# Kernel tuning notes

Hardware: AMD Instinct MI355X
Metric: run time of the kernel (lower is better)

Reference implementation:

```python
import jax, jax.numpy as jnp
import numpy as np

N_TYPES = 4
N_REL = 8
N_HEADS = 8
IN_DIM = 256
N_HID = 128
D_K = N_HID // N_HEADS
N_LAYERS = 2
N_NODES = 100000
N_EDGES = 400000


def setup_inputs() -> dict:
    key = jax.random.key(0)
    ks = jax.random.split(key, 24)
    s = 0.05
    inp = {
        'node_feature': jax.random.normal(ks[0], (N_NODES, IN_DIM), jnp.float32),
        'node_type': jax.random.randint(ks[1], (N_NODES,), 0, N_TYPES),
        'edge_index': jax.random.randint(ks[2], (2, N_EDGES), 0, N_NODES),
        'edge_type': jax.random.randint(ks[3], (N_EDGES,), 0, N_REL),
        # per-type input adapters
        'adapt_w': jax.random.normal(ks[4], (N_TYPES, IN_DIM, N_HID), jnp.float32) * s,
        'adapt_b': jnp.zeros((N_TYPES, N_HID), jnp.float32),
        # HGT conv params, stacked over layers
        'k_w': jax.random.normal(ks[5], (N_LAYERS, N_TYPES, N_HID, N_HID), jnp.float32) * s,
        'k_b': jnp.zeros((N_LAYERS, N_TYPES, N_HID), jnp.float32),
        'q_w': jax.random.normal(ks[6], (N_LAYERS, N_TYPES, N_HID, N_HID), jnp.float32) * s,
        'q_b': jnp.zeros((N_LAYERS, N_TYPES, N_HID), jnp.float32),
        'v_w': jax.random.normal(ks[7], (N_LAYERS, N_TYPES, N_HID, N_HID), jnp.float32) * s,
        'v_b': jnp.zeros((N_LAYERS, N_TYPES, N_HID), jnp.float32),
        'a_w': jax.random.normal(ks[8], (N_LAYERS, N_TYPES, N_HID, N_HID), jnp.float32) * s,
        'a_b': jnp.zeros((N_LAYERS, N_TYPES, N_HID), jnp.float32),
        'rel_pri': jnp.ones((N_LAYERS, N_REL, N_HEADS), jnp.float32),
        'rel_att': jnp.tile(jnp.eye(D_K, dtype=jnp.float32), (N_LAYERS, N_REL, N_HEADS, 1, 1))
                   + jax.random.normal(ks[9], (N_LAYERS, N_REL, N_HEADS, D_K, D_K), jnp.float32) * s,
        'rel_msg': jnp.tile(jnp.eye(D_K, dtype=jnp.float32), (N_LAYERS, N_REL, N_HEADS, 1, 1))
                   + jax.random.normal(ks[10], (N_LAYERS, N_REL, N_HEADS, D_K, D_K), jnp.float32) * s,
        'skip': jnp.ones((N_LAYERS, N_TYPES), jnp.float32),
    }
    return inp


def _per_type_linear(x, w, b, node_type, n_idx):
    # x: [N, din], w: [T, din, dout], b: [T, dout] -> gather row for each node's type
    h_all = jnp.einsum('ni,tio->tno', x, w) + b[:, None, :]  # [T, N, dout]
    return h_all[node_type, n_idx]  # [N, dout]


def _edge_softmax(score, tgt, n):
    # score: [E, H]; softmax over incoming edges of each target node
    m = jax.ops.segment_max(score, tgt, num_segments=n)  # [N, H]
    e = jnp.exp(score - m[tgt])
    z = jax.ops.segment_sum(e, tgt, num_segments=n)
    return e / (z[tgt] + 1e-9)


def _hgt_layer(x, node_type, src, tgt, edge_type,
               kw, kb, qw, qb, vw, vb, aw, ab, pri, att_m, msg_m, skip):
    n = x.shape[0]
    n_idx = jnp.arange(n)
    k = _per_type_linear(x, kw, kb, node_type, n_idx).reshape(n, N_HEADS, D_K)
    q = _per_type_linear(x, qw, qb, node_type, n_idx).reshape(n, N_HEADS, D_K)
    v = _per_type_linear(x, vw, vb, node_type, n_idx).reshape(n, N_HEADS, D_K)
    k_src, v_src, q_tgt = k[src], v[src], q[tgt]  # [E, H, dk]
    # per-relation attention/message transforms, accumulated over small fixed R
    k_rel = jnp.zeros_like(k_src)
    v_rel = jnp.zeros_like(v_src)
    for r in range(N_REL):
        msk = (edge_type == r)[:, None, None]
        k_rel = k_rel + jnp.einsum('ehd,hdf->ehf', jnp.where(msk, k_src, 0.0), att_m[r])
        v_rel = v_rel + jnp.einsum('ehd,hdf->ehf', jnp.where(msk, v_src, 0.0), msg_m[r])
    score = (q_tgt * k_rel).sum(-1) * pri[edge_type] * (1.0 / (D_K ** 0.5))  # [E, H]
    att = _edge_softmax(score, tgt, n)
    agg = jax.ops.segment_sum(att[..., None] * v_rel, tgt, num_segments=n)  # [N, H, dk]
    agg = agg.reshape(n, N_HID)
    trans = _per_type_linear(jax.nn.gelu(agg), aw, ab, node_type, n_idx)
    alpha = jax.nn.sigmoid(skip)[node_type][:, None]
    return trans * alpha + x * (1.0 - alpha)


def reference(node_feature, node_type, edge_index, edge_type,
              adapt_w, adapt_b, k_w, k_b, q_w, q_b, v_w, v_b,
              a_w, a_b, rel_pri, rel_att, rel_msg, skip):
    n = node_feature.shape[0]
    n_idx = jnp.arange(n)
    # per-node-type adapter + tanh (gather-linear-scatter, fully vectorized)
    h = jnp.tanh(_per_type_linear(node_feature, adapt_w, adapt_b, node_type, n_idx))
    src, tgt = edge_index[0], edge_index[1]
    for l in range(N_LAYERS):
        h = _hgt_layer(h, node_type, src, tgt, edge_type,
                       k_w[l], k_b[l], q_w[l], q_b[l], v_w[l], v_b[l],
                       a_w[l], a_b[l], rel_pri[l], rel_att[l], rel_msg[l], skip[l])
    return h
```

## Files before the change

### kernel.cpp

```cpp
#include <hip/hip_runtime.h>
#include <hip/hip_fp16.h>
#include <math.h>

constexpr int N_TYPES = 4;
constexpr int N_REL   = 8;
constexpr int N_HEADS = 8;
constexpr int IN_DIM  = 256;
constexpr int N_HID   = 128;
constexpr int D_K     = 16;
constexpr int N_LAYERS= 2;
constexpr int NN      = 100000;
constexpr int NE      = 400000;
constexpr int NBLK    = (NN + 255) / 256;

typedef _Float16 f16x8 __attribute__((ext_vector_type(8)));
typedef float    f32x4 __attribute__((ext_vector_type(4)));

__device__ __forceinline__ float gelu_f(float x) {
    const float c = 0.7978845608028654f;
    float x3 = x * x * x;
    return 0.5f * x * (1.0f + tanhf(c * (x + 0.044715f * x3)));
}
__device__ __forceinline__ float sigmoid_f(float x) {
    return 1.0f / (1.0f + expf(-x));
}

__global__ __launch_bounds__(256) void count2_kernel(
    const int* __restrict__ ntype, const int* __restrict__ tgt,
    unsigned* ncnt, unsigned* tcnt)
{
    int i = blockIdx.x * 256 + threadIdx.x;
    int lane = threadIdx.x & 63;
    int t = (i < NN) ? ntype[i] : -1;
    #pragma unroll
    for (int tt = 0; tt < N_TYPES; tt++) {
        unsigned long long m = __ballot(t == tt);
        if (m != 0ull && lane == __ffsll((unsigned long long)m) - 1)
            atomicAdd(&ncnt[tt], (unsigned)__popcll(m));
    }
    if (i < NE) atomicAdd(&tcnt[tgt[i]], 1u);
}

__global__ void node_offsets_kernel(unsigned* c)
{
    unsigned a = 0;
    for (int t = 0; t < N_TYPES; t++) { c[8 + t] = a; c[4 + t] = a; a += c[t]; }
    c[8 + N_TYPES] = a;
}

__global__ __launch_bounds__(256) void scan1_kernel(
    const unsigned* __restrict__ cnt, unsigned* __restrict__ eoff,
    unsigned* __restrict__ bsum)
{
    __shared__ unsigned sh[256];
    int i = blockIdx.x * 256 + threadIdx.x;
    unsigned v = (i < NN) ? cnt[i] : 0u;
    sh[threadIdx.x] = v;
    __syncthreads();
    for (int off = 1; off < 256; off <<= 1) {
        unsigned add = (threadIdx.x >= off) ? sh[threadIdx.x - off] : 0u;
        __syncthreads();
        sh[threadIdx.x] += add;
        __syncthreads();
    }
    if (i < NN) eoff[i] = sh[threadIdx.x] - v;
    if (threadIdx.x == 255) bsum[blockIdx.x] = sh[255];
}

__global__ __launch_bounds__(512) void scan2_kernel(unsigned* __restrict__ bsum)
{
    __shared__ unsigned sh[512];
    int i = threadIdx.x;
    unsigned v = (i < NBLK) ? bsum[i] : 0u;
    sh[i] = v;
    __syncthreads();
    for (int off = 1; off < 512; off <<= 1) {
        unsigned add = (i >= off) ? sh[i - off] : 0u;
        __syncthreads();
        sh[i] += add;
        __syncthreads();
    }
    if (i < NBLK) bsum[i] = sh[i] - v;
}

__global__ __launch_bounds__(256) void scan3_kernel(
    unsigned* __restrict__ eoff, const unsigned* __restrict__ bsum,
    unsigned* __restrict__ ecur)
{
    int i = blockIdx.x * 256 + threadIdx.x;
    if (i < NN) {
        unsigned v = eoff[i] + bsum[blockIdx.x];
        eoff[i] = v;
        ecur[i] = v;
    }
    if (i == 0) eoff[NN] = (unsigned)NE;
}

__global__ __launch_bounds__(256) void scatter2_kernel(
    const int* __restrict__ ntype,
    const int* __restrict__ src, const int* __restrict__ tgt,
    const int* __restrict__ etype,
    unsigned* ncur, unsigned* ecur,
    int* __restrict__ nidx,
    int* __restrict__ er_t)
{
    int i = blockIdx.x * 256 + threadIdx.x;
    int lane = threadIdx.x & 63;
    int t = (i < NN) ? ntype[i] : -1;
    #pragma unroll
    for (int tt = 0; tt < N_TYPES; tt++) {
        unsigned long long m = __ballot(t == tt);
        if (m == 0ull) continue;
        int leader = __ffsll((unsigned long long)m) - 1;
        unsigned base = 0;
        if (lane == leader) base = atomicAdd(&ncur[tt], (unsigned)__popcll(m));
        base = __shfl(base, leader, 64);
        if (t == tt) {
            unsigned rank = (unsigned)__popcll(m & ((1ull << lane) - 1ull));
            nidx[base + rank] = i;
        }
    }
    if (i < NE) {
        int tg = tgt[i];
        unsigned p = atomicAdd(&ecur[tg], 1u);
        er_t[p] = (src[i] << 3) | etype[i];
    }
}

__global__ __launch_bounds__(256) void cvt_w_layers_kernel(
    const float* __restrict__ kw, const float* __restrict__ qw,
    const float* __restrict__ vw, const float* __restrict__ aw,
    __half* __restrict__ whT)
{
    int gid = blockIdx.x * 256 + threadIdx.x;
    constexpr int per = 2 * 4 * 128 * 128;
    if (gid >= 4 * per) return;
    int m = gid >> 17;
    int rem = gid & (per - 1);
    const float* W = (m == 0) ? kw : (m == 1) ? qw : (m == 2) ? vw : aw;
    float val = W[rem];
    int l = rem >> 16;
    int r2 = rem & 65535;
    int t = r2 >> 14;
    int r3 = r2 & 16383;
    int k = r3 >> 7, n = r3 & 127;
    whT[((size_t)(l * 4 + m) << 16) + ((size_t)t << 14) + (n << 7) + k] =
        __float2half(val);
}

__global__ __launch_bounds__(256) void cvt_wA_kernel(
    const float* __restrict__ W, __half* __restrict__ whT)
{
    int gid = blockIdx.x * 256 + threadIdx.x;
    if (gid >= 4 * 256 * 128) return;
    int t = gid >> 15;
    int rem = gid & 32767;
    int k = rem >> 7, n = rem & 127;
    whT[((size_t)t * 128 + n) * 256 + k] = __float2half(W[gid]);
}

template<int DIN, int F32IN, int MOUT, int OH>
__global__ __launch_bounds__(256) void mfma_ptl_kernel(
    const void* __restrict__ x,
    const int* __restrict__ nidx, const unsigned* __restrict__ noff,
    const __half* __restrict__ whT,
    const float* __restrict__ Bb,
    const float* __restrict__ skipv, const __half* __restrict__ hprev,
    void* __restrict__ out)
{
    const int t = blockIdx.y;
    const unsigned s0 = noff[t], s1 = noff[t + 1];
    const unsigned base = s0 + blockIdx.x * 128u;
    if (base >= s1) return;
    const int nrows = (int)min(128u, s1 - base);

    __shared__ __align__(16) ushort xsh[128][40];
    __shared__ __align__(16) ushort wsh[128][40];
    __shared__ int nid[128];

    const int tid = threadIdx.x;
    if (tid < 128) nid[tid] = nidx[base + (unsigned)min(tid, nrows - 1)];
    __syncthreads();

    const int lane = tid & 63;
    const int wave = tid >> 6;
    const int wr = wave >> 1, wc = wave & 1;
    const int lm = lane & 15, lk = lane >> 4;

    f32x4 acc[4][4];
    #pragma unroll
    for (int a = 0; a < 4; a++)
        #pragma unroll
        for (int b = 0; b < 4; b++)
            acc[a][b] = (f32x4){0.0f, 0.0f, 0.0f, 0.0f};

    const ushort* WT = (const ushort*)whT + (size_t)t * 128 * DIN;
    const int srow = tid & 127, shalf = tid >> 7;
    const size_t xoff = (size_t)nid[srow] * DIN;

    for (int k0 = 0; k0 < DIN; k0 += 32) {
        if (F32IN) {
            const float* xp = (const float*)x + xoff + k0 + shalf * 16;
            float4 a0 = ((const float4*)xp)[0];
            float4 a1 = ((const float4*)xp)[1];
            float4 a2 = ((const float4*)xp)[2];
            float4 a3 = ((const float4*)xp)[3];
            float v[16] = {a0.x, a0.y, a0.z, a0.w, a1.x, a1.y, a1.z, a1.w,
                           a2.x, a2.y, a2.z, a2.w, a3.x, a3.y, a3.z, a3.w};
            __align__(16) __half hh[16];
            #pragma unroll
            for (int i = 0; i < 16; i++) hh[i] = __float2half(v[i]);
            *(uint4*)&xsh[srow][shalf * 16]     = ((uint4*)hh)[0];
            *(uint4*)&xsh[srow][shalf * 16 + 8] = ((uint4*)hh)[1];
        } else {
            const ushort* ph = (const ushort*)x + xoff + k0 + shalf * 16;
            *(uint4*)&xsh[srow][shalf * 16]     = *(const uint4*)ph;
            *(uint4*)&xsh[srow][shalf * 16 + 8] = *(const uint4*)(ph + 8);
        }
        {
            const ushort* qh = WT + (size_t)srow * DIN + k0 + shalf * 16;
            *(uint4*)&wsh[srow][shalf * 16]     = *(const uint4*)qh;
            *(uint4*)&wsh[srow][shalf * 16 + 8] = *(const uint4*)(qh + 8);
        }
        __syncthreads();
        f16x8 ah[4];
        #pragma unroll
        for (int fm = 0; fm < 4; fm++)
            ah[fm] = *(const f16x8*)&xsh[wr * 64 + fm * 16 + lm][lk * 8];
        #pragma unroll
        for (int fn = 0; fn < 4; fn++) {
            f16x8 bh = *(const f16x8*)&wsh[wc * 64 + fn * 16 + lm][lk * 8];
            #pragma unroll
            for (int fm = 0; fm < 4; fm++)
                acc[fm][fn] = __builtin_amdgcn_mfma_f32_16x16x32_f16(
                    ah[fm], bh, acc[fm][fn], 0, 0, 0);
        }
        __syncthreads();
    }

    float alpha = 0.0f;
    if (MOUT == 2) alpha = sigmoid_f(skipv[t]);
    #pragma unroll
    for (int fn = 0; fn < 4; fn++) {
        const int dim = wc * 64 + fn * 16 + lm;
        const float bias = Bb[t * 128 + dim];
        #pragma unroll
        for (int fm = 0; fm < 4; fm++) {
            #pragma unroll
            for (int i = 0; i < 4; i++) {
                int rr = wr * 64 + fm * 16 + lk * 4 + i;
                if (rr < nrows) {
                    int n = nid[rr];
                    float o = acc[fm][fn][i] + bias;
                    if (MOUT == 0) o = tanhf(o);
                    else if (MOUT == 2)
                        o = o * alpha +
                            __half2float(hprev[(size_t)n * 128 + dim]) * (1.0f - alpha);
                    if (OH == 0) ((float*)out)[(size_t)n * 128 + dim] = o;
                    else ((__half*)out)[(size_t)n * 128 + dim] = __float2half(o);
                }
            }
        }
    }
}

__global__ __launch_bounds__(256) void mfma_kqv_kernel(
    const __half* __restrict__ xh,
    const int* __restrict__ nidx, const unsigned* __restrict__ noff,
    const __half* __restrict__ wTk, const float* __restrict__ bk, __half* __restrict__ ok,
    const __half* __restrict__ wTq, const float* __restrict__ bq, __half* __restrict__ oq,
    const __half* __restrict__ wTv, const float* __restrict__ bv, __half* __restrict__ ov)
{
    const int t = blockIdx.y;
    const unsigned s0 = noff[t], s1 = noff[t + 1];
    const unsigned base = s0 + blockIdx.x * 128u;
    if (base >= s1) return;
    const int nrows = (int)min(128u, s1 - base);

    __shared__ __align__(16) ushort xsh[128][136];
    __shared__ __align__(16) ushort wsh[128][40];
    __shared__ int nid[128];

    const int tid = threadIdx.x;
    if (tid < 128) nid[tid] = nidx[base + (unsigned)min(tid, nrows - 1)];
    __syncthreads();

    const int srow = tid & 127, shalf = tid >> 7;
    {
        const ushort* xp = (const ushort*)xh + (size_t)nid[srow] * 128 + shalf * 64;
        #pragma unroll
        for (int i = 0; i < 8; i++)
            *(uint4*)&xsh[srow][shalf * 64 + i * 8] = ((const uint4*)xp)[i];
    }

    const int lane = tid & 63;
    const int wave = tid >> 6;
    const int wr = wave >> 1, wc = wave & 1;
    const int lm = lane & 15, lk = lane >> 4;

    const ushort* WTs[3] = { (const ushort*)wTk + ((size_t)t << 14),
                             (const ushort*)wTq + ((size_t)t << 14),
                             (const ushort*)wTv + ((size_t)t << 14) };
    const float* Bs[3] = { bk, bq, bv };
    __half* Os[3] = { ok, oq, ov };

    #pragma unroll
    for (int w = 0; w < 3; w++) {
        f32x4 acc[4][4];
        #pragma unroll
        for (int a = 0; a < 4; a++)
            #pragma unroll
            for (int b = 0; b < 4; b++)
                acc[a][b] = (f32x4){0.0f, 0.0f, 0.0f, 0.0f};

        for (int k0 = 0; k0 < 128; k0 += 32) {
            __syncthreads();
            {
                const ushort* qh = WTs[w] + ((size_t)srow << 7) + k0 + shalf * 16;
                *(uint4*)&wsh[srow][shalf * 16]     = *(const uint4*)qh;
                *(uint4*)&wsh[srow][shalf * 16 + 8] = *(const uint4*)(qh + 8);
            }
            __syncthreads();
            f16x8 ah[4];
            #pragma unroll
            for (int fm = 0; fm < 4; fm++)
                ah[fm] = *(const f16x8*)&xsh[wr * 64 + fm * 16 + lm][k0 + lk * 8];
            #pragma unroll
            for (int fn = 0; fn < 4; fn++) {
                f16x8 bh = *(const f16x8*)&wsh[wc * 64 + fn * 16 + lm][lk * 8];
                #pragma unroll
                for (int fm = 0; fm < 4; fm++)
                    acc[fm][fn] = __builtin_amdgcn_mfma_f32_16x16x32_f16(
                        ah[fm], bh, acc[fm][fn], 0, 0, 0);
            }
        }
        #pragma unroll
        for (int fn = 0; fn < 4; fn++) {
            const int dim = wc * 64 + fn * 16 + lm;
            const float bias = Bs[w][t * 128 + dim];
            #pragma unroll
            for (int fm = 0; fm < 4; fm++) {
                #pragma unroll
                for (int i = 0; i < 4; i++) {
                    int rr = wr * 64 + fm * 16 + lk * 4 + i;
                    if (rr < nrows) {
                        int n = nid[rr];
                        Os[w][(size_t)n * 128 + dim] =
                            __float2half(acc[fm][fn][i] + bias);
                    }
                }
            }
        }
    }
}

__global__ __launch_bounds__(256) void hgt_edge_fused(
    const int* __restrict__ er_t,
    const unsigned* __restrict__ eoff,
    const __half* __restrict__ kh,
    const __half* __restrict__ vh,
    const float* __restrict__ att,
    const float* __restrict__ msg,
    const float* __restrict__ pri,
    __half* __restrict__ qagg)
{
    __shared__ float aq_lds[2][1024];
    __shared__ float pv_lds[2][1024];
    const int tid  = threadIdx.x;
    const int tsel = tid >> 7;
    const int li   = tid & 127;
    const int h    = li >> 4;
    const int j    = li & 15;
    const int l    = tid & 63;
    const int hb   = tid & 0x30;
    const int t    = blockIdx.x * 2 + tsel;
    if (t >= NN) return;

    const unsigned e0 = eoff[t];
    const unsigned e1 = eoff[t + 1];
    const int deg = (int)(e1 - e0);

    if (deg == 0) {
        qagg[(size_t)t * 128 + li] = __float2half(0.0f);
        return;
    }

    float* al = aq_lds[tsel];
    float* pl = pv_lds[tsel];

    #pragma unroll
    for (int r = 0; r < 8; r++) pl[r * 128 + li] = 0.0f;

    const float qo = __half2float(qagg[(size_t)t * 128 + li]);
    float qh[16];
    #pragma unroll
    for (int f = 0; f < 16; f++) qh[f] = __shfl(qo, hb + f, 64);

    int pkl = 0;
    if (l < 16 && e0 + (unsigned)l < e1) pkl = er_t[e0 + l];

    const int dc = min(deg, 16);
    unsigned mask = 0;
    for (int c = 0; c < dc; ++c) mask |= 1u << (__shfl(pkl, c, 64) & 7);
    for (unsigned e = e0 + 16; e < e1; ++e) mask |= 1u << (er_t[e] & 7);

    unsigned need = mask;
    while (need) {
        const int r = __ffs(need) - 1; need &= need - 1;
        const float* Ar = att + (((r * 8 + h) * 16 + j) * 16);
        float4 A0 = ((const float4*)Ar)[0];
        float4 A1 = ((const float4*)Ar)[1];
        float4 A2 = ((const float4*)Ar)[2];
        float4 A3 = ((const float4*)Ar)[3];
        float acc =
            A0.x*qh[0]  + A0.y*qh[1]  + A0.z*qh[2]  + A0.w*qh[3]  +
            A1.x*qh[4]  + A1.y*qh[5]  + A1.z*qh[6]  + A1.w*qh[7]  +
            A2.x*qh[8]  + A2.y*qh[9]  + A2.z*qh[10] + A2.w*qh[11] +
            A3.x*qh[12] + A3.y*qh[13] + A3.z*qh[14] + A3.w*qh[15];
        al[r * 128 + li] = acc * pri[r * 8 + h] * 0.25f;
    }

    float z = 0.0f;
    float* plp = pl + li;
    const float* alp = al + li;
    const __half* kb = kh + li;
    const __half* vb = vh + li;

    unsigned e = e0;
    for (; e + 4 <= e1; e += 4) {
        const int o = (int)(e - e0);
        int p0, p1, p2, p3;
        if (o + 3 < 16) {
            p0 = __shfl(pkl, o + 0, 64);
            p1 = __shfl(pkl, o + 1, 64);
            p2 = __shfl(pkl, o + 2, 64);
            p3 = __shfl(pkl, o + 3, 64);
        } else {
            p0 = er_t[e + 0]; p1 = er_t[e + 1];
            p2 = er_t[e + 2]; p3 = er_t[e + 3];
        }
        const int o0 = (p0 & ~7) << 4;
        const int o1 = (p1 & ~7) << 4;
        const int o2 = (p2 & ~7) << 4;
        const int o3 = (p3 & ~7) << 4;
        const float k0 = __half2float(kb[o0]); const float v0 = __half2float(vb[o0]);
        const float k1 = __half2float(kb[o1]); const float v1 = __half2float(vb[o1]);
        const float k2 = __half2float(kb[o2]); const float v2 = __half2float(vb[o2]);
        const float k3 = __half2float(kb[o3]); const float v3 = __half2float(vb[o3]);
        float s0 = k0 * alp[(p0 & 7) * 128];
        float s1 = k1 * alp[(p1 & 7) * 128];
        float s2 = k2 * alp[(p2 & 7) * 128];
        float s3 = k3 * alp[(p3 & 7) * 128];
        s0 += __shfl_xor(s0, 1); s1 += __shfl_xor(s1, 1);
        s2 += __shfl_xor(s2, 1); s3 += __shfl_xor(s3, 1);
        s0 += __shfl_xor(s0, 2); s1 += __shfl_xor(s1, 2);
        s2 += __shfl_xor(s2, 2); s3 += __shfl_xor(s3, 2);
        s0 += __shfl_xor(s0, 4); s1 += __shfl_xor(s1, 4);
        s2 += __shfl_xor(s2, 4); s3 += __shfl_xor(s3, 4);
        s0 += __shfl_xor(s0, 8); s1 += __shfl_xor(s1, 8);
        s2 += __shfl_xor(s2, 8); s3 += __shfl_xor(s3, 8);
        const float q0 = __expf(s0 - 8.0f);
        const float q1 = __expf(s1 - 8.0f);
        const float q2 = __expf(s2 - 8.0f);
        const float q3 = __expf(s3 - 8.0f);
        z += q0 + q1 + q2 + q3;
        plp[(p0 & 7) * 128] += q0 * v0;
        plp[(p1 & 7) * 128] += q1 * v1;
        plp[(p2 & 7) * 128] += q2 * v2;
        plp[(p3 & 7) * 128] += q3 * v3;
    }
    if (e + 2 <= e1) {
        const int o = (int)(e - e0);
        int p0, p1;
        if (o + 1 < 16) { p0 = __shfl(pkl, o, 64); p1 = __shfl(pkl, o + 1, 64); }
        else            { p0 = er_t[e]; p1 = er_t[e + 1]; }
        const int o0 = (p0 & ~7) << 4;
        const int o1 = (p1 & ~7) << 4;
        const float k0 = __half2float(kb[o0]); const float v0 = __half2float(vb[o0]);
        const float k1 = __half2float(kb[o1]); const float v1 = __half2float(vb[o1]);
        float s0 = k0 * alp[(p0 & 7) * 128];
        float s1 = k1 * alp[(p1 & 7) * 128];
        s0 += __shfl_xor(s0, 1); s1 += __shfl_xor(s1, 1);
        s0 += __shfl_xor(s0, 2); s1 += __shfl_xor(s1, 2);
        s0 += __shfl_xor(s0, 4); s1 += __shfl_xor(s1, 4);
        s0 += __shfl_xor(s0, 8); s1 += __shfl_xor(s1, 8);
        const float q0 = __expf(s0 - 8.0f);
        const float q1 = __expf(s1 - 8.0f);
        z += q0 + q1;
        plp[(p0 & 7) * 128] += q0 * v0;
        plp[(p1 & 7) * 128] += q1 * v1;
        e += 2;
    }
    if (e < e1) {
        const int o = (int)(e - e0);
        const int p0 = (o < 16) ? __shfl(pkl, o, 64) : er_t[e];
        const int o0 = (p0 & ~7) << 4;
        const float k0 = __half2float(kb[o0]); const float v0 = __half2float(vb[o0]);
        float s0 = k0 * alp[(p0 & 7) * 128];
        s0 += __shfl_xor(s0, 1);
        s0 += __shfl_xor(s0, 2);
        s0 += __shfl_xor(s0, 4);
        s0 += __shfl_xor(s0, 8);
        const float q0 = __expf(s0 - 8.0f);
        z += q0;
        plp[(p0 & 7) * 128] += q0 * v0;
    }

    float acc = 0.0f;
    for (int r = 0; r < 8; r++) {
        if (!((mask >> r) & 1)) continue;
        const float* Mr = msg + ((r * 8 + h) * 256) + j;
        const float* sb = pl + r * 128 + h * 16;
        #pragma unroll
        for (int d = 0; d < 16; d++)
            acc += sb[d] * Mr[d * 16];
    }
    qagg[(size_t)t * 128 + li] =
        __float2half(gelu_f(acc * __frcp_rn(z + 1e-9f)));
}

extern "C" void kernel_launch(void* const* d_in, const int* in_sizes, int n_in,
                              void* d_out, int out_size, void* d_ws, size_t ws_size,
                              hipStream_t stream)
{
    const float* node_feature = (const float*)d_in[0];
    const int*   node_type    = (const int*)d_in[1];
    const int*   edge_index   = (const int*)d_in[2];
    const int*   edge_type    = (const int*)d_in[3];
    const float* adapt_w      = (const float*)d_in[4];
    const float* adapt_b      = (const float*)d_in[5];
    const float* k_w = (const float*)d_in[6];
    const float* k_b = (const float*)d_in[7];
    const float* q_w = (const float*)d_in[8];
    const float* q_b = (const float*)d_in[9];
    const float* v_w = (const float*)d_in[10];
    const float* v_b = (const float*)d_in[11];
    const float* a_w = (const float*)d_in[12];
    const float* a_b = (const float*)d_in[13];
    const float* rel_pri = (const float*)d_in[14];
    const float* rel_att = (const float*)d_in[15];
    const float* rel_msg = (const float*)d_in[16];
    const float* skip    = (const float*)d_in[17];

    const int* src = edge_index;
    const int* tgt = edge_index + NE;

    float* OUT = (float*)d_out;

    char* w = (char*)d_ws;
    auto alloc = [&](size_t bytes) -> void* {
        void* p = (void*)w;
        w += (bytes + 255) & ~(size_t)255;
        return p;
    };
    __half*   H0    = (__half*)alloc((size_t)NN * 128 * 2);
    __half*   H1    = (__half*)alloc((size_t)NN * 128 * 2);
    __half*   KH    = (__half*)alloc((size_t)NN * 128 * 2);
    __half*   VH    = (__half*)alloc((size_t)NN * 128 * 2);
    __half*   QA    = (__half*)alloc((size_t)NN * 128 * 2);
    __half*   WHT   = (__half*)alloc((size_t)8 * 4 * 128 * 128 * 2);
    __half*   WAT   = (__half*)alloc((size_t)4 * 128 * 256 * 2);
    int*      nidx  = (int*)alloc((size_t)NN * 4);
    int*      er_t  = (int*)alloc((size_t)NE * 4);
    unsigned* tcnt  = (unsigned*)alloc((size_t)NN * 4);
    unsigned* eoff  = (unsigned*)alloc((size_t)(NN + 1) * 4);
    unsigned* ecur  = (unsigned*)alloc((size_t)NN * 4);
    unsigned* bsum  = (unsigned*)alloc((size_t)NBLK * 4);
    unsigned* cnts  = (unsigned*)alloc(16 * 4);

    unsigned* ncnt = cnts;
    unsigned* ncur = cnts + 4;
    unsigned* noff = cnts + 8;

    hipMemsetAsync(cnts, 0, 16 * 4, stream);
    hipMemsetAsync(tcnt, 0, (size_t)NN * 4, stream);

    const int gblocks = (NE + 255) / 256;
    count2_kernel<<<gblocks, 256, 0, stream>>>(node_type, tgt, ncnt, tcnt);
    node_offsets_kernel<<<1, 1, 0, stream>>>(cnts);
    scan1_kernel<<<NBLK, 256, 0, stream>>>(tcnt, eoff, bsum);
    scan2_kernel<<<1, 512, 0, stream>>>(bsum);
    scan3_kernel<<<NBLK, 256, 0, stream>>>(eoff, bsum, ecur);
    scatter2_kernel<<<gblocks, 256, 0, stream>>>(node_type, src, tgt, edge_type,
                                                 ncur, ecur, nidx, er_t);

    cvt_w_layers_kernel<<<(4 * 2 * 4 * 128 * 128 + 255) / 256, 256, 0, stream>>>(
        k_w, q_w, v_w, a_w, WHT);
    cvt_wA_kernel<<<(4 * 256 * 128 + 255) / 256, 256, 0, stream>>>(adapt_w, WAT);

    dim3 pgrid((NN + 127) / 128, N_TYPES);
    mfma_ptl_kernel<IN_DIM, 1, 0, 1><<<pgrid, 256, 0, stream>>>(
        node_feature, nidx, noff, WAT, adapt_b, nullptr, nullptr, H0);

    const int fblocks = (NN + 1) / 2;
    const size_t wtot = (size_t)4 * 128 * 128;

    for (int l = 0; l < N_LAYERS; l++) {
        __half* hin = l ? H1 : H0;

        const __half* khT = WHT + (size_t)(l * 4 + 0) * wtot;
        const __half* qhT = WHT + (size_t)(l * 4 + 1) * wtot;
        const __half* vhT = WHT + (size_t)(l * 4 + 2) * wtot;
        const __half* ahT = WHT + (size_t)(l * 4 + 3) * wtot;

        const float* kbl = k_b + (size_t)l * N_TYPES * 128;
        const float* qbl = q_b + (size_t)l * N_TYPES * 128;
        const float* vbl = v_b + (size_t)l * N_TYPES * 128;
        const float* abl = a_b + (size_t)l * N_TYPES * 128;
        const float* pril = rel_pri + (size_t)l * N_REL * N_HEADS;
        const float* attl = rel_att + (size_t)l * N_REL * N_HEADS * D_K * D_K;
        const float* msgl = rel_msg + (size_t)l * N_REL * N_HEADS * D_K * D_K;
        const float* skipl = skip + (size_t)l * N_TYPES;

        mfma_kqv_kernel<<<pgrid, 256, 0, stream>>>(
            hin, nidx, noff,
            khT, kbl, KH,
            qhT, qbl, QA,
            vhT, vbl, VH);

        hgt_edge_fused<<<fblocks, 256, 0, stream>>>(
            er_t, eoff, KH, VH, attl, msgl, pril, QA);

        if (l == 0)
            mfma_ptl_kernel<N_HID, 0, 2, 1><<<pgrid, 256, 0, stream>>>(
                QA, nidx, noff, ahT, abl, skipl, H0, H1);
        else
            mfma_ptl_kernel<N_HID, 0, 2, 0><<<pgrid, 256, 0, stream>>>(
                QA, nidx, noff, ahT, abl, skipl, H1, OUT);
    }
}
```

Baseline: 1.024 ms.

## Store first eight edges per node inline and prescale attention by priority

The scatter step now writes each target's first eight packed edges into a fixed-stride per-node buffer, and only overflow edges go into the CSR array. This lets the edge kernel load them at once, without first waiting on the eoff offsets. The relation attention matrices are pre-multiplied by the relation priority and the 1/sqrt(d_k) factor in a small setup kernel, which removes a load and multiply from the per-relation loop. The node-offset computation is folded into scan2, which saves one launch. The cost is an extra 3.2MB buffer plus a memset for the per-node cursors.

```diff
diff --git a/kernel.cpp b/kernel.cpp
--- a/kernel.cpp
+++ b/kernel.cpp
@@ -41,13 +41,6 @@
     if (i < NE) atomicAdd(&tcnt[tgt[i]], 1u);
 }
 
-__global__ void node_offsets_kernel(unsigned* c)
-{
-    unsigned a = 0;
-    for (int t = 0; t < N_TYPES; t++) { c[8 + t] = a; c[4 + t] = a; a += c[t]; }
-    c[8 + N_TYPES] = a;
-}
-
 __global__ __launch_bounds__(256) void scan1_kernel(
     const unsigned* __restrict__ cnt, unsigned* __restrict__ eoff,
     unsigned* __restrict__ bsum)
@@ -67,10 +60,16 @@
     if (threadIdx.x == 255) bsum[blockIdx.x] = sh[255];
 }
 
-__global__ __launch_bounds__(512) void scan2_kernel(unsigned* __restrict__ bsum)
+__global__ __launch_bounds__(512) void scan2_kernel(
+    unsigned* __restrict__ bsum, unsigned* __restrict__ c)
 {
     __shared__ unsigned sh[512];
     int i = threadIdx.x;
+    if (i == 0) {
+        unsigned a = 0;
+        for (int t = 0; t < N_TYPES; t++) { c[8 + t] = a; c[4 + t] = a; a += c[t]; }
+        c[8 + N_TYPES] = a;
+    }
     unsigned v = (i < NBLK) ? bsum[i] : 0u;
     sh[i] = v;
     __syncthreads();
@@ -84,15 +83,10 @@
 }
 
 __global__ __launch_bounds__(256) void scan3_kernel(
-    unsigned* __restrict__ eoff, const unsigned* __restrict__ bsum,
-    unsigned* __restrict__ ecur)
+    unsigned* __restrict__ eoff, const unsigned* __restrict__ bsum)
 {
     int i = blockIdx.x * 256 + threadIdx.x;
-    if (i < NN) {
-        unsigned v = eoff[i] + bsum[blockIdx.x];
-        eoff[i] = v;
-        ecur[i] = v;
-    }
+    if (i < NN) eoff[i] += bsum[blockIdx.x];
     if (i == 0) eoff[NN] = (unsigned)NE;
 }
 
@@ -100,9 +94,9 @@
     const int* __restrict__ ntype,
     const int* __restrict__ src, const int* __restrict__ tgt,
     const int* __restrict__ etype,
-    unsigned* ncur, unsigned* ecur,
+    unsigned* ncur, unsigned* ecur0, const unsigned* __restrict__ eoff,
     int* __restrict__ nidx,
-    int* __restrict__ er_t)
+    int* __restrict__ pk8, int* __restrict__ er_t)
 {
     int i = blockIdx.x * 256 + threadIdx.x;
     int lane = threadIdx.x & 63;
@@ -122,9 +116,21 @@
     }
     if (i < NE) {
         int tg = tgt[i];
-        unsigned p = atomicAdd(&ecur[tg], 1u);
-        er_t[p] = (src[i] << 3) | etype[i];
-    }
+        int pk = (src[i] << 3) | etype[i];
+        unsigned slot = atomicAdd(&ecur0[tg], 1u);
+        if (slot < 8) pk8[tg * 8 + slot] = pk;
+        else          er_t[eoff[tg] + slot] = pk;
+    }
+}
+
+__global__ __launch_bounds__(256) void prescale_att_kernel(
+    const float* __restrict__ att, const float* __restrict__ pri,
+    float* __restrict__ attS)
+{
+    int gid = blockIdx.x * 256 + threadIdx.x;
+    if (gid >= N_LAYERS * N_REL * N_HEADS * 256) return;
+    int lrh = gid >> 8;
+    attS[gid] = att[gid] * pri[lrh] * 0.25f;
 }
 
 __global__ __launch_bounds__(256) void cvt_w_layers_kernel(
@@ -355,13 +361,13 @@
 }
 
 __global__ __launch_bounds__(256) void hgt_edge_fused(
+    const int* __restrict__ pk8,
     const int* __restrict__ er_t,
     const unsigned* __restrict__ eoff,
     const __half* __restrict__ kh,
     const __half* __restrict__ vh,
-    const float* __restrict__ att,
+    const float* __restrict__ attS,
     const float* __restrict__ msg,
-    const float* __restrict__ pri,
     __half* __restrict__ qagg)
 {
     __shared__ float aq_lds[2][1024];
@@ -376,10 +382,13 @@
     const int t    = blockIdx.x * 2 + tsel;
     if (t >= NN) return;
 
+    int pkl = 0;
+    if (l < 8) pkl = pk8[t * 8 + l];
     const unsigned e0 = eoff[t];
     const unsigned e1 = eoff[t + 1];
+    const float qo = __half2float(qagg[(size_t)t * 128 + li]);
+
     const int deg = (int)(e1 - e0);
-
     if (deg == 0) {
         qagg[(size_t)t * 128 + li] = __float2half(0.0f);
         return;
@@ -391,33 +400,28 @@
     #pragma unroll
     for (int r = 0; r < 8; r++) pl[r * 128 + li] = 0.0f;
 
-    const float qo = __half2float(qagg[(size_t)t * 128 + li]);
     float qh[16];
     #pragma unroll
     for (int f = 0; f < 16; f++) qh[f] = __shfl(qo, hb + f, 64);
 
-    int pkl = 0;
-    if (l < 16 && e0 + (unsigned)l < e1) pkl = er_t[e0 + l];
-
-    const int dc = min(deg, 16);
+    const int dc = min(deg, 8);
     unsigned mask = 0;
     for (int c = 0; c < dc; ++c) mask |= 1u << (__shfl(pkl, c, 64) & 7);
-    for (unsigned e = e0 + 16; e < e1; ++e) mask |= 1u << (er_t[e] & 7);
+    for (unsigned e = e0 + 8; e < e1; ++e) mask |= 1u << (er_t[e] & 7);
 
     unsigned need = mask;
     while (need) {
         const int r = __ffs(need) - 1; need &= need - 1;
-        const float* Ar = att + (((r * 8 + h) * 16 + j) * 16);
+        const float* Ar = attS + (((r * 8 + h) * 16 + j) * 16);
         float4 A0 = ((const float4*)Ar)[0];
         float4 A1 = ((const float4*)Ar)[1];
         float4 A2 = ((const float4*)Ar)[2];
         float4 A3 = ((const float4*)Ar)[3];
-        float acc =
+        al[r * 128 + li] =
             A0.x*qh[0]  + A0.y*qh[1]  + A0.z*qh[2]  + A0.w*qh[3]  +
             A1.x*qh[4]  + A1.y*qh[5]  + A1.z*qh[6]  + A1.w*qh[7]  +
             A2.x*qh[8]  + A2.y*qh[9]  + A2.z*qh[10] + A2.w*qh[11] +
             A3.x*qh[12] + A3.y*qh[13] + A3.z*qh[14] + A3.w*qh[15];
-        al[r * 128 + li] = acc * pri[r * 8 + h] * 0.25f;
     }
 
     float z = 0.0f;
@@ -430,7 +434,7 @@
     for (; e + 4 <= e1; e += 4) {
         const int o = (int)(e - e0);
         int p0, p1, p2, p3;
-        if (o + 3 < 16) {
+        if (o + 3 < 8) {
             p0 = __shfl(pkl, o + 0, 64);
             p1 = __shfl(pkl, o + 1, 64);
             p2 = __shfl(pkl, o + 2, 64);
@@ -472,8 +476,8 @@
     if (e + 2 <= e1) {
         const int o = (int)(e - e0);
         int p0, p1;
-        if (o + 1 < 16) { p0 = __shfl(pkl, o, 64); p1 = __shfl(pkl, o + 1, 64); }
-        else            { p0 = er_t[e]; p1 = er_t[e + 1]; }
+        if (o + 1 < 8) { p0 = __shfl(pkl, o, 64); p1 = __shfl(pkl, o + 1, 64); }
+        else           { p0 = er_t[e]; p1 = er_t[e + 1]; }
         const int o0 = (p0 & ~7) << 4;
         const int o1 = (p1 & ~7) << 4;
         const float k0 = __half2float(kb[o0]); const float v0 = __half2float(vb[o0]);
@@ -493,7 +497,7 @@
     }
     if (e < e1) {
         const int o = (int)(e - e0);
-        const int p0 = (o < 16) ? __shfl(pkl, o, 64) : er_t[e];
+        const int p0 = (o < 8) ? __shfl(pkl, o, 64) : er_t[e];
         const int o0 = (p0 & ~7) << 4;
         const float k0 = __half2float(kb[o0]); const float v0 = __half2float(vb[o0]);
         float s0 = k0 * alp[(p0 & 7) * 128];
@@ -560,11 +564,13 @@
     __half*   QA    = (__half*)alloc((size_t)NN * 128 * 2);
     __half*   WHT   = (__half*)alloc((size_t)8 * 4 * 128 * 128 * 2);
     __half*   WAT   = (__half*)alloc((size_t)4 * 128 * 256 * 2);
+    float*    attS  = (float*)alloc((size_t)N_LAYERS * 64 * 256 * 4);
     int*      nidx  = (int*)alloc((size_t)NN * 4);
+    int*      pk8   = (int*)alloc((size_t)NN * 8 * 4);
     int*      er_t  = (int*)alloc((size_t)NE * 4);
     unsigned* tcnt  = (unsigned*)alloc((size_t)NN * 4);
     unsigned* eoff  = (unsigned*)alloc((size_t)(NN + 1) * 4);
-    unsigned* ecur  = (unsigned*)alloc((size_t)NN * 4);
+    unsigned* ecur0 = (unsigned*)alloc((size_t)NN * 4);
     unsigned* bsum  = (unsigned*)alloc((size_t)NBLK * 4);
     unsigned* cnts  = (unsigned*)alloc(16 * 4);
 
@@ -574,19 +580,21 @@
 
     hipMemsetAsync(cnts, 0, 16 * 4, stream);
     hipMemsetAsync(tcnt, 0, (size_t)NN * 4, stream);
+    hipMemsetAsync(ecur0, 0, (size_t)NN * 4, stream);
 
     const int gblocks = (NE + 255) / 256;
     count2_kernel<<<gblocks, 256, 0, stream>>>(node_type, tgt, ncnt, tcnt);
-    node_offsets_kernel<<<1, 1, 0, stream>>>(cnts);
     scan1_kernel<<<NBLK, 256, 0, stream>>>(tcnt, eoff, bsum);
-    scan2_kernel<<<1, 512, 0, stream>>>(bsum);
-    scan3_kernel<<<NBLK, 256, 0, stream>>>(eoff, bsum, ecur);
+    scan2_kernel<<<1, 512, 0, stream>>>(bsum, cnts);
+    scan3_kernel<<<NBLK, 256, 0, stream>>>(eoff, bsum);
     scatter2_kernel<<<gblocks, 256, 0, stream>>>(node_type, src, tgt, edge_type,
-                                                 ncur, ecur, nidx, er_t);
+                                                 ncur, ecur0, eoff, nidx, pk8, er_t);
 
     cvt_w_layers_kernel<<<(4 * 2 * 4 * 128 * 128 + 255) / 256, 256, 0, stream>>>(
         k_w, q_w, v_w, a_w, WHT);
     cvt_wA_kernel<<<(4 * 256 * 128 + 255) / 256, 256, 0, stream>>>(adapt_w, WAT);
+    prescale_att_kernel<<<(N_LAYERS * 64 * 256 + 255) / 256, 256, 0, stream>>>(
+        rel_att, rel_pri, attS);
 
     dim3 pgrid((NN + 127) / 128, N_TYPES);
     mfma_ptl_kernel<IN_DIM, 1, 0, 1><<<pgrid, 256, 0, stream>>>(
@@ -607,8 +615,7 @@
         const float* qbl = q_b + (size_t)l * N_TYPES * 128;
         const float* vbl = v_b + (size_t)l * N_TYPES * 128;
         const float* abl = a_b + (size_t)l * N_TYPES * 128;
-        const float* pril = rel_pri + (size_t)l * N_REL * N_HEADS;
-        const float* attl = rel_att + (size_t)l * N_REL * N_HEADS * D_K * D_K;
+        const float* attSl = attS + (size_t)l * 64 * 256;
         const float* msgl = rel_msg + (size_t)l * N_REL * N_HEADS * D_K * D_K;
         const float* skipl = skip + (size_t)l * N_TYPES;
 
@@ -619,7 +626,7 @@
             vhT, vbl, VH);
 
         hgt_edge_fused<<<fblocks, 256, 0, stream>>>(
-            er_t, eoff, KH, VH, attl, msgl, pril, QA);
+            pk8, er_t, eoff, KH, VH, attSl, msgl, QA);
 
         if (l == 0)
             mfma_ptl_kernel<N_HID, 0, 2, 1><<<pgrid, 256, 0, stream>>>(
```

Measured after the change: 1.032 ms. No clear change (+0.8%).
